# Kernel tuning notes

Hardware: AMD Instinct MI355X
Metric: run time of the kernel (lower is better)

The kernel has to match this reference:

```python
import jax, jax.numpy as jnp
import numpy as np

SEG = 2048      # segment_length
RATE = 4        # dilated_rate
DIM = 768
LN_EPS = 1e-5


def _sparsify(x):
    # b (l s) d -> b l s d, take every RATE-th within segment, flatten back
    b, L, d = x.shape
    x = x.reshape(b, L // SEG, SEG, d)[:, :, ::RATE]
    return x.reshape(b, -1, d)


def _layernorm(x, gamma, beta):
    mu = jnp.mean(x, axis=-1, keepdims=True)
    var = jnp.mean(jnp.square(x - mu), axis=-1, keepdims=True)
    return (x - mu) / jnp.sqrt(var + LN_EPS) * gamma + beta


def setup_inputs() -> dict:
    key = jax.random.key(0)
    ks = jax.random.split(key, 6)
    B, L, D = 4, 8192, DIM
    return {
        "Q": jax.random.normal(ks[0], (B, L, D), dtype=jnp.float32),
        "K": jax.random.normal(ks[1], (B, L, D), dtype=jnp.float32),
        "V": jax.random.normal(ks[2], (B, L, D), dtype=jnp.float32),
        "Wq": jax.random.normal(ks[3], (D, D), dtype=jnp.float32) * (1.0 / np.sqrt(D)),
        "Wk": jax.random.normal(ks[4], (D, D), dtype=jnp.float32) * (1.0 / np.sqrt(D)),
        "Wv": jax.random.normal(ks[5], (D, D), dtype=jnp.float32) * (1.0 / np.sqrt(D)),
        "ln_gamma": jnp.ones((D,), dtype=jnp.float32),
        "ln_beta": jnp.zeros((D,), dtype=jnp.float32),
    }


def reference(Q, K, V, Wq, Wk, Wv, ln_gamma, ln_beta):
    # strided segment dilation gather
    q = _sparsify(Q)  # [B, Ls, D], Ls = L/SEG * ceil(SEG/RATE)
    k = _sparsify(K)
    v = _sparsify(V)
    # linear projections (torch Linear: y = x @ W.T, no bias)
    q = q @ Wq.T
    k = k @ Wk.T
    v = v @ Wv.T
    # qk LayerNorm (shared norm module)
    q = _layernorm(q, ln_gamma, ln_beta)
    k = _layernorm(k, ln_gamma, ln_beta)
    # scaled dot product attention (non-causal, default scale 1/sqrt(D))
    scale = 1.0 / np.sqrt(q.shape[-1]).astype(np.float32)
    attn = jax.nn.softmax(jnp.einsum('bqd,bkd->bqk', q, k) * scale, axis=-1)
    out = jnp.einsum('bqk,bkd->bqd', attn, v)
    # dropout is identity in eval mode; final softmax over feature dim (as in source)
    return jax.nn.softmax(out, axis=-1)
```

## Files before the change

### kernel.cpp

```cpp
#include <hip/hip_runtime.h>
#include <math.h>

#define SEGLEN 2048
#define SRATE 4
#define DIM 768
#define BATCH 4
#define LFULL 8192
#define LSP 2048
#define NROWS (BATCH * LSP)
#define LN_EPS 1e-5f
#define ATT_SCALE 0.03608439182435161f

typedef __attribute__((ext_vector_type(8))) short s16x8;
typedef __attribute__((ext_vector_type(4))) float f32x4;

__device__ __forceinline__ ushort f2bf(float f) {
    unsigned u = __float_as_uint(f);
    u += 0x7fffu + ((u >> 16) & 1u);
    return (ushort)(u >> 16);
}
__device__ __forceinline__ float bf2f(ushort h) {
    return __uint_as_float(((unsigned)h) << 16);
}

__device__ __forceinline__ void ld_lds16(const ushort* g, ushort* l) {
    __builtin_amdgcn_global_load_lds(
        (const __attribute__((address_space(1))) void*)g,
        (__attribute__((address_space(3))) void*)l, 16, 0, 0);
}

__global__ void pack3(const float* __restrict__ Q, const float* __restrict__ Ks,
                      const float* __restrict__ V, ushort* __restrict__ X) {
    const float* src = blockIdx.z == 0 ? Q : blockIdx.z == 1 ? Ks : V;
    ushort* dst = X + (long)blockIdx.z * (NROWS * DIM);
    int idx = blockIdx.x * 256 + threadIdx.x;
    int r  = idx / (DIM / 4);
    int dg = idx - r * (DIM / 4);
    int bb = r >> 11;
    int s  = r & 2047;
    int seg = s >> 9;
    int j   = s & 511;
    long srow = (long)bb * LFULL + seg * SEGLEN + j * SRATE;
    float4 f = *(const float4*)(src + srow * DIM + dg * 4);
    ushort4 o;
    o.x = f2bf(f.x); o.y = f2bf(f.y); o.z = f2bf(f.z); o.w = f2bf(f.w);
    *(ushort4*)(dst + (long)r * DIM + dg * 4) = o;
}

__global__ void conv3(const float* __restrict__ Wq, const float* __restrict__ Wk,
                      const float* __restrict__ Wv, ushort* __restrict__ W) {
    const float* src = blockIdx.z == 0 ? Wq : blockIdx.z == 1 ? Wk : Wv;
    ushort* dst = W + (long)blockIdx.z * (DIM * DIM);
    int idx = blockIdx.x * 256 + threadIdx.x;
    float4 f = *(const float4*)(src + (long)idx * 4);
    ushort4 o;
    o.x = f2bf(f.x); o.y = f2bf(f.y); o.z = f2bf(f.z); o.w = f2bf(f.w);
    *(ushort4*)(dst + (long)idx * 4) = o;
}

template<int MODE>
__global__ __launch_bounds__(512, 2) void gemm8(
    const ushort* __restrict__ Ag, const ushort* __restrict__ Bg,
    ushort* __restrict__ Cb, ushort* __restrict__ Cb2,
    float* __restrict__ Cf, float* __restrict__ Cf2, float* __restrict__ lsum,
    int M, int N, int K, int lda, int ldb, long sA, long sB, long sC,
    int ldc, float scale)
{
    __shared__ ushort lds[2][2][16384];

    const int z = blockIdx.z;
    const int bz = (MODE == 3) ? (z >> 1) : z;
    const int hz = (MODE == 3) ? (z & 1) : 0;
    const ushort* Aop = Ag + (long)bz * sA + (long)hz * K;
    const ushort* Bop = Bg + (long)bz * sB + (long)hz * K;

    const int tid = threadIdx.x;
    const int w = tid >> 6, lane = tid & 63;
    const int wm = w >> 2, wn = w & 3;
    const int quad = lane >> 4, lr = lane & 15;
    const int rowBase = blockIdx.y * 256;
    const int colBase = blockIdx.x * 256;

    int ib = ((lane & 15) << 6) | ((lane >> 4) << 4);
    ib ^= ((ib >> 9) & 1) << 5;

    long offA[4], offB[4];
#pragma unroll
    for (int i = 0; i < 4; i++) {
        int c = i * 512 + tid;
        int cc = c ^ (((c >> 5) & 1) << 1);
        int s = cc >> 6;
        int row  = ((s >> 1) << 4) + ((cc >> 2) & 15);
        int colE = ((s & 1) << 5) + ((cc & 3) << 3);
        offA[i] = (long)(rowBase + row) * lda + colE;
        offB[i] = (long)(colBase + row) * ldb + colE;
    }

    const int NT = K >> 6;

#define STA(buf, vv, i) ld_lds16(Aop + offA[i] + (long)(vv) * 64, &lds[buf][0][(i) * 4096 + w * 512])
#define STB(buf, vv, i) ld_lds16(Bop + offB[i] + (long)(vv) * 64, &lds[buf][1][(i) * 4096 + w * 512])

#pragma unroll
    for (int i = 0; i < 4; i++) STB(0, 0, i);
#pragma unroll
    for (int i = 0; i < 4; i++) STA(0, 0, i);
#pragma unroll
    for (int i = 0; i < 4; i++) STB(1, 1, i);
#pragma unroll
    for (int i = 0; i < 4; i++) STA(1, 1, i);
    asm volatile("s_waitcnt vmcnt(8)" ::: "memory");
    __builtin_amdgcn_s_barrier();

    f32x4 acc[8][4] = {};
    s16x8 bq[4][2];

    for (int v = 0; v < NT; ++v) {
        const int b = v & 1;
        const char* lA = (const char*)&lds[b][0][0];
        const char* lB = (const char*)&lds[b][1][0];
#pragma unroll
        for (int p = 0; p < 4; ++p) {
            s16x8 aq[2][2];
#pragma unroll
            for (int t = 0; t < 2; ++t)
#pragma unroll
                for (int ks = 0; ks < 2; ++ks)
                    aq[t][ks] = *(const s16x8*)(lA + (((wm * 8 + p * 2 + t) * 2 + ks) << 10) + ib);
            if (p == 0) {
#pragma unroll
                for (int n = 0; n < 4; ++n)
#pragma unroll
                    for (int ks = 0; ks < 2; ++ks)
                        bq[n][ks] = *(const s16x8*)(lB + (((wn * 4 + n) * 2 + ks) << 10) + ib);
            }
            if (p == 0 && v >= 1 && v + 1 < NT) { STA(b ^ 1, v + 1, 0); STA(b ^ 1, v + 1, 1); }
            if (p == 1 && v >= 1 && v + 1 < NT) { STA(b ^ 1, v + 1, 2); STA(b ^ 1, v + 1, 3); }
            if (p == 2 && v + 2 < NT)           { STB(b,     v + 2, 0); STB(b,     v + 2, 1); }
            if (p == 3 && v + 2 < NT)           { STB(b,     v + 2, 2); STB(b,     v + 2, 3); }

            __builtin_amdgcn_s_barrier();
            __builtin_amdgcn_s_setprio(1);
#pragma unroll
            for (int t = 0; t < 2; ++t)
#pragma unroll
                for (int n = 0; n < 4; ++n)
#pragma unroll
                    for (int ks = 0; ks < 2; ++ks)
                        acc[p * 2 + t][n] = __builtin_amdgcn_mfma_f32_16x16x32_bf16(
                            aq[t][ks], bq[n][ks], acc[p * 2 + t][n], 0, 0, 0);
            __builtin_amdgcn_s_setprio(0);
            if (p == 3) {
                if (v + 2 < NT)      asm volatile("s_waitcnt vmcnt(4)" ::: "memory");
                else if (v + 1 < NT) asm volatile("s_waitcnt vmcnt(0)" ::: "memory");
            }
            __builtin_amdgcn_s_barrier();
        }
    }
#undef STA
#undef STB

    if (MODE == 0) {
        if (z < 2) {
            ushort* Cz = Cb + (long)z * sC;
#pragma unroll
            for (int i = 0; i < 8; i++) {
                int r0 = rowBase + wm * 128 + i * 16 + quad * 4;
#pragma unroll
                for (int j = 0; j < 4; j++) {
                    int c = colBase + wn * 64 + j * 16 + lr;
#pragma unroll
                    for (int reg = 0; reg < 4; reg++)
                        Cz[(long)(r0 + reg) * ldc + c] = f2bf(acc[i][j][reg]);
                }
            }
        } else {
#pragma unroll
            for (int i = 0; i < 8; i++) {
                int r0 = rowBase + wm * 128 + i * 16 + quad * 4;
                int bidx = r0 >> 11;
                int jj = r0 & 2047;
                ushort* Cz = Cb2 + (long)bidx * DIM * LSP;
#pragma unroll
                for (int j = 0; j < 4; j++) {
                    int c = colBase + wn * 64 + j * 16 + lr;
                    ushort4 o;
                    o.x = f2bf(acc[i][j][0]); o.y = f2bf(acc[i][j][1]);
                    o.z = f2bf(acc[i][j][2]); o.w = f2bf(acc[i][j][3]);
                    *(ushort4*)(Cz + (long)c * LSP + jj) = o;
                }
            }
        }
    } else if (MODE == 2) {
        ushort* Cz = Cb + (long)z * sC;
        float* lz = lsum + (long)z * M;
#pragma unroll
        for (int i = 0; i < 8; i++) {
            int r0 = rowBase + wm * 128 + i * 16 + quad * 4;
#pragma unroll
            for (int reg = 0; reg < 4; reg++) {
                float s = 0.f;
#pragma unroll
                for (int j = 0; j < 4; j++) {
                    int c = colBase + wn * 64 + j * 16 + lr;
                    float e = __expf(acc[i][j][reg] * scale);
                    s += e;
                    Cz[(long)(r0 + reg) * ldc + c] = f2bf(e);
                }
                for (int m = 1; m < 16; m <<= 1) s += __shfl_xor(s, m, 64);
                if (lr == 0) atomicAdd(&lz[r0 + reg], s);
            }
        }
    } else {
        float* Cz = (hz ? Cf2 : Cf) + (long)bz * sC;
#pragma unroll
        for (int i = 0; i < 8; i++) {
            int r0 = rowBase + wm * 128 + i * 16 + quad * 4;
#pragma unroll
            for (int j = 0; j < 4; j++) {
                int c = colBase + wn * 64 + j * 16 + lr;
#pragma unroll
                for (int reg = 0; reg < 4; reg++)
                    Cz[(long)(r0 + reg) * ldc + c] = acc[i][j][reg];
            }
        }
    }
}

__global__ __launch_bounds__(256) void ln_inplace(
    ushort* __restrict__ X, const float* __restrict__ gamma,
    const float* __restrict__ beta)
{
    int wid = threadIdx.x >> 6, lane = threadIdx.x & 63;
    int row = blockIdx.x * 4 + wid;
    ushort* xp = X + (long)row * DIM;
    float v[12];
    float s = 0.f;
#pragma unroll
    for (int c = 0; c < 12; c++) { v[c] = bf2f(xp[c * 64 + lane]); s += v[c]; }
    for (int m = 1; m < 64; m <<= 1) s += __shfl_xor(s, m, 64);
    float mean = s * (1.0f / 768.0f);
    float q = 0.f;
#pragma unroll
    for (int c = 0; c < 12; c++) { float d = v[c] - mean; q += d * d; }
    for (int m = 1; m < 64; m <<= 1) q += __shfl_xor(q, m, 64);
    float rstd = rsqrtf(q * (1.0f / 768.0f) + LN_EPS);
#pragma unroll
    for (int c = 0; c < 12; c++) {
        int idx = c * 64 + lane;
        float y = (v[c] - mean) * rstd * gamma[idx] + beta[idx];
        xp[idx] = f2bf(y);
    }
}

__global__ __launch_bounds__(256) void final_softmax(
    const float* __restrict__ O0, const float* __restrict__ O1,
    const float* __restrict__ l, float* __restrict__ out)
{
    int wid = threadIdx.x >> 6, lane = threadIdx.x & 63;
    int row = blockIdx.x * 4 + wid;
    long base = (long)row * DIM;
    float inv = 1.0f / l[row];
    float v[12]; float mx = -1e30f;
#pragma unroll
    for (int c = 0; c < 12; c++) {
        v[c] = (O0[base + c * 64 + lane] + O1[base + c * 64 + lane]) * inv;
        mx = fmaxf(mx, v[c]);
    }
    for (int m = 1; m < 64; m <<= 1) mx = fmaxf(mx, __shfl_xor(mx, m, 64));
    float s = 0.f;
#pragma unroll
    for (int c = 0; c < 12; c++) { v[c] = __expf(v[c] - mx); s += v[c]; }
    for (int m = 1; m < 64; m <<= 1) s += __shfl_xor(s, m, 64);
    float invs = 1.0f / s;
#pragma unroll
    for (int c = 0; c < 12; c++) out[base + c * 64 + lane] = v[c] * invs;
}

extern "C" void kernel_launch(void* const* d_in, const int* in_sizes, int n_in,
                              void* d_out, int out_size, void* d_ws, size_t ws_size,
                              hipStream_t stream)
{
    const float* Q  = (const float*)d_in[0];
    const float* K_ = (const float*)d_in[1];
    const float* V  = (const float*)d_in[2];
    const float* Wq = (const float*)d_in[3];
    const float* Wk = (const float*)d_in[4];
    const float* Wv = (const float*)d_in[5];
    const float* g  = (const float*)d_in[6];
    const float* b  = (const float*)d_in[7];
    float* out = (float*)d_out;

    char* ws = (char*)d_ws;
    ushort* Xq  = (ushort*)(ws + 0);
    ushort* Wqb = (ushort*)(ws + 37748736);
    ushort* qb  = (ushort*)(ws + 41287680);
    ushort* kb  = (ushort*)(ws + 53870592);
    ushort* vT  = (ushort*)(ws + 66453504);
    float*  O0  = (float*)(ws + 79036416);
    float*  l   = (float*)(ws + 104202240);
    ushort* P   = (ushort*)(ws + 0);
    float*  O1  = (float*)(ws + 41287680);

    (void)in_sizes; (void)n_in; (void)out_size; (void)ws_size;

    hipMemsetAsync(l, 0, NROWS * sizeof(float), stream);

    pack3<<<dim3(6144, 1, 3), 256, 0, stream>>>(Q, K_, V, Xq);
    conv3<<<dim3(576, 1, 3), 256, 0, stream>>>(Wq, Wk, Wv, Wqb);

    gemm8<0><<<dim3(DIM / 256, NROWS / 256, 3), 512, 0, stream>>>(
        Xq, Wqb, qb, vT, nullptr, nullptr, nullptr,
        NROWS, DIM, DIM, DIM, DIM,
        (long)NROWS * DIM, (long)DIM * DIM, (long)NROWS * DIM, DIM, 0.f);

    ln_inplace<<<4096, 256, 0, stream>>>(qb, g, b);

    gemm8<2><<<dim3(LSP / 256, LSP / 256, BATCH), 512, 0, stream>>>(
        qb, kb, P, nullptr, nullptr, nullptr, l,
        LSP, LSP, DIM, DIM, DIM,
        (long)LSP * DIM, (long)LSP * DIM, (long)LSP * LSP, LSP, ATT_SCALE);

    gemm8<3><<<dim3(DIM / 256, LSP / 256, BATCH * 2), 512, 0, stream>>>(
        P, vT, nullptr, nullptr, O0, O1, nullptr,
        LSP, DIM, LSP / 2, LSP, LSP,
        (long)LSP * LSP, (long)DIM * LSP, (long)LSP * DIM, DIM, 0.f);

    final_softmax<<<2048, 256, 0, stream>>>(O0, O1, l, out);
}
```

Before: 395.8 us.

## Shrink GEMM tiles to 128x128 with simpler double buffering and XCD-aware block remap

Replaces the 256x256, 8-wave GEMM tile with a 128x128, 4-wave tile and a simpler pipeline that prefetches the next K-slice at the start of each iteration and waits once at the end. It also remaps the flattened block index round-robin across eight groups, apparently to spread neighbouring tiles across the MI355X's XCDs for L2 locality. The aim is more workgroups to fill the CUs, since the grids were small, and less scheduling complexity. In exchange, each tile reuses data less and does more global and LDS loading per FLOP, and the interleaved A/B prefetch schedule is lost.

```diff
diff --git a/kernel.cpp b/kernel.cpp
--- a/kernel.cpp
+++ b/kernel.cpp
@@ -59,27 +59,35 @@
 }
 
 template<int MODE>
-__global__ __launch_bounds__(512, 2) void gemm8(
+__global__ __launch_bounds__(256, 2) void gemm_bt(
     const ushort* __restrict__ Ag, const ushort* __restrict__ Bg,
     ushort* __restrict__ Cb, ushort* __restrict__ Cb2,
     float* __restrict__ Cf, float* __restrict__ Cf2, float* __restrict__ lsum,
     int M, int N, int K, int lda, int ldb, long sA, long sB, long sC,
     int ldc, float scale)
 {
-    __shared__ ushort lds[2][2][16384];
-
-    const int z = blockIdx.z;
+    __shared__ ushort lds[2][2][8192];
+
+    const int gx = gridDim.x, gy = gridDim.y;
+    const int G = gx * gy * gridDim.z;
+    const int f = blockIdx.x + gx * (blockIdx.y + gy * blockIdx.z);
+    const int wg = (f & 7) * (G >> 3) + (f >> 3);
+    const int bx = wg % gx;
+    const int rest = wg / gx;
+    const int by = rest % gy;
+    const int z  = rest / gy;
+
     const int bz = (MODE == 3) ? (z >> 1) : z;
     const int hz = (MODE == 3) ? (z & 1) : 0;
     const ushort* Aop = Ag + (long)bz * sA + (long)hz * K;
     const ushort* Bop = Bg + (long)bz * sB + (long)hz * K;
 
     const int tid = threadIdx.x;
-    const int w = tid >> 6, lane = tid & 63;
-    const int wm = w >> 2, wn = w & 3;
+    const int wid = tid >> 6, lane = tid & 63;
+    const int wm = wid >> 1, wn = wid & 1;
     const int quad = lane >> 4, lr = lane & 15;
-    const int rowBase = blockIdx.y * 256;
-    const int colBase = blockIdx.x * 256;
+    const int rowBase = by * 128;
+    const int colBase = bx * 128;
 
     int ib = ((lane & 15) << 6) | ((lane >> 4) << 4);
     ib ^= ((ib >> 9) & 1) << 5;
@@ -87,7 +95,7 @@
     long offA[4], offB[4];
 #pragma unroll
     for (int i = 0; i < 4; i++) {
-        int c = i * 512 + tid;
+        int c = i * 256 + tid;
         int cc = c ^ (((c >> 5) & 1) << 1);
         int s = cc >> 6;
         int row  = ((s >> 1) << 4) + ((cc >> 2) & 15);
@@ -98,64 +106,44 @@
 
     const int NT = K >> 6;
 
-#define STA(buf, vv, i) ld_lds16(Aop + offA[i] + (long)(vv) * 64, &lds[buf][0][(i) * 4096 + w * 512])
-#define STB(buf, vv, i) ld_lds16(Bop + offB[i] + (long)(vv) * 64, &lds[buf][1][(i) * 4096 + w * 512])
-
-#pragma unroll
-    for (int i = 0; i < 4; i++) STB(0, 0, i);
-#pragma unroll
-    for (int i = 0; i < 4; i++) STA(0, 0, i);
-#pragma unroll
-    for (int i = 0; i < 4; i++) STB(1, 1, i);
-#pragma unroll
-    for (int i = 0; i < 4; i++) STA(1, 1, i);
-    asm volatile("s_waitcnt vmcnt(8)" ::: "memory");
+#define STA(buf, vv, i) ld_lds16(Aop + offA[i] + (long)(vv) * 64, &lds[buf][0][(i) * 2048 + wid * 512])
+#define STB(buf, vv, i) ld_lds16(Bop + offB[i] + (long)(vv) * 64, &lds[buf][1][(i) * 2048 + wid * 512])
+
+#pragma unroll
+    for (int i = 0; i < 4; i++) { STA(0, 0, i); STB(0, 0, i); }
+    asm volatile("s_waitcnt vmcnt(0)" ::: "memory");
     __builtin_amdgcn_s_barrier();
 
-    f32x4 acc[8][4] = {};
-    s16x8 bq[4][2];
+    f32x4 acc[4][4] = {};
 
     for (int v = 0; v < NT; ++v) {
         const int b = v & 1;
+        if (v + 1 < NT) {
+#pragma unroll
+            for (int i = 0; i < 4; i++) { STA(b ^ 1, v + 1, i); STB(b ^ 1, v + 1, i); }
+        }
         const char* lA = (const char*)&lds[b][0][0];
         const char* lB = (const char*)&lds[b][1][0];
 #pragma unroll
-        for (int p = 0; p < 4; ++p) {
-            s16x8 aq[2][2];
-#pragma unroll
-            for (int t = 0; t < 2; ++t)
-#pragma unroll
-                for (int ks = 0; ks < 2; ++ks)
-                    aq[t][ks] = *(const s16x8*)(lA + (((wm * 8 + p * 2 + t) * 2 + ks) << 10) + ib);
-            if (p == 0) {
-#pragma unroll
-                for (int n = 0; n < 4; ++n)
-#pragma unroll
-                    for (int ks = 0; ks < 2; ++ks)
-                        bq[n][ks] = *(const s16x8*)(lB + (((wn * 4 + n) * 2 + ks) << 10) + ib);
-            }
-            if (p == 0 && v >= 1 && v + 1 < NT) { STA(b ^ 1, v + 1, 0); STA(b ^ 1, v + 1, 1); }
-            if (p == 1 && v >= 1 && v + 1 < NT) { STA(b ^ 1, v + 1, 2); STA(b ^ 1, v + 1, 3); }
-            if (p == 2 && v + 2 < NT)           { STB(b,     v + 2, 0); STB(b,     v + 2, 1); }
-            if (p == 3 && v + 2 < NT)           { STB(b,     v + 2, 2); STB(b,     v + 2, 3); }
-
-            __builtin_amdgcn_s_barrier();
+        for (int ks = 0; ks < 2; ++ks) {
+            s16x8 af[4], bfm[4];
+#pragma unroll
+            for (int t = 0; t < 4; ++t)
+                af[t] = *(const s16x8*)(lA + (((wm * 4 + t) * 2 + ks) << 10) + ib);
+#pragma unroll
+            for (int t = 0; t < 4; ++t)
+                bfm[t] = *(const s16x8*)(lB + (((wn * 4 + t) * 2 + ks) << 10) + ib);
             __builtin_amdgcn_s_setprio(1);
 #pragma unroll
-            for (int t = 0; t < 2; ++t)
-#pragma unroll
-                for (int n = 0; n < 4; ++n)
-#pragma unroll
-                    for (int ks = 0; ks < 2; ++ks)
-                        acc[p * 2 + t][n] = __builtin_amdgcn_mfma_f32_16x16x32_bf16(
-                            aq[t][ks], bq[n][ks], acc[p * 2 + t][n], 0, 0, 0);
+            for (int i = 0; i < 4; i++)
+#pragma unroll
+                for (int j = 0; j < 4; j++)
+                    acc[i][j] = __builtin_amdgcn_mfma_f32_16x16x32_bf16(
+                        af[i], bfm[j], acc[i][j], 0, 0, 0);
             __builtin_amdgcn_s_setprio(0);
-            if (p == 3) {
-                if (v + 2 < NT)      asm volatile("s_waitcnt vmcnt(4)" ::: "memory");
-                else if (v + 1 < NT) asm volatile("s_waitcnt vmcnt(0)" ::: "memory");
-            }
-            __builtin_amdgcn_s_barrier();
-        }
+        }
+        if (v + 1 < NT) asm volatile("s_waitcnt vmcnt(0)" ::: "memory");
+        __builtin_amdgcn_s_barrier();
     }
 #undef STA
 #undef STB
@@ -164,8 +152,8 @@
         if (z < 2) {
             ushort* Cz = Cb + (long)z * sC;
 #pragma unroll
-            for (int i = 0; i < 8; i++) {
-                int r0 = rowBase + wm * 128 + i * 16 + quad * 4;
+            for (int i = 0; i < 4; i++) {
+                int r0 = rowBase + wm * 64 + i * 16 + quad * 4;
 #pragma unroll
                 for (int j = 0; j < 4; j++) {
                     int c = colBase + wn * 64 + j * 16 + lr;
@@ -176,8 +164,8 @@
             }
         } else {
 #pragma unroll
-            for (int i = 0; i < 8; i++) {
-                int r0 = rowBase + wm * 128 + i * 16 + quad * 4;
+            for (int i = 0; i < 4; i++) {
+                int r0 = rowBase + wm * 64 + i * 16 + quad * 4;
                 int bidx = r0 >> 11;
                 int jj = r0 & 2047;
                 ushort* Cz = Cb2 + (long)bidx * DIM * LSP;
@@ -195,8 +183,8 @@
         ushort* Cz = Cb + (long)z * sC;
         float* lz = lsum + (long)z * M;
 #pragma unroll
-        for (int i = 0; i < 8; i++) {
-            int r0 = rowBase + wm * 128 + i * 16 + quad * 4;
+        for (int i = 0; i < 4; i++) {
+            int r0 = rowBase + wm * 64 + i * 16 + quad * 4;
 #pragma unroll
             for (int reg = 0; reg < 4; reg++) {
                 float s = 0.f;
@@ -214,8 +202,8 @@
     } else {
         float* Cz = (hz ? Cf2 : Cf) + (long)bz * sC;
 #pragma unroll
-        for (int i = 0; i < 8; i++) {
-            int r0 = rowBase + wm * 128 + i * 16 + quad * 4;
+        for (int i = 0; i < 4; i++) {
+            int r0 = rowBase + wm * 64 + i * 16 + quad * 4;
 #pragma unroll
             for (int j = 0; j < 4; j++) {
                 int c = colBase + wn * 64 + j * 16 + lr;
@@ -309,19 +297,19 @@
     pack3<<<dim3(6144, 1, 3), 256, 0, stream>>>(Q, K_, V, Xq);
     conv3<<<dim3(576, 1, 3), 256, 0, stream>>>(Wq, Wk, Wv, Wqb);
 
-    gemm8<0><<<dim3(DIM / 256, NROWS / 256, 3), 512, 0, stream>>>(
+    gemm_bt<0><<<dim3(DIM / 128, NROWS / 128, 3), 256, 0, stream>>>(
         Xq, Wqb, qb, vT, nullptr, nullptr, nullptr,
         NROWS, DIM, DIM, DIM, DIM,
         (long)NROWS * DIM, (long)DIM * DIM, (long)NROWS * DIM, DIM, 0.f);
 
     ln_inplace<<<4096, 256, 0, stream>>>(qb, g, b);
 
-    gemm8<2><<<dim3(LSP / 256, LSP / 256, BATCH), 512, 0, stream>>>(
+    gemm_bt<2><<<dim3(LSP / 128, LSP / 128, BATCH), 256, 0, stream>>>(
         qb, kb, P, nullptr, nullptr, nullptr, l,
         LSP, LSP, DIM, DIM, DIM,
         (long)LSP * DIM, (long)LSP * DIM, (long)LSP * LSP, LSP, ATT_SCALE);
 
-    gemm8<3><<<dim3(DIM / 256, LSP / 256, BATCH * 2), 512, 0, stream>>>(
+    gemm_bt<3><<<dim3(DIM / 128, LSP / 128, BATCH * 2), 256, 0, stream>>>(
         P, vT, nullptr, nullptr, O0, O1, nullptr,
         LSP, DIM, LSP / 2, LSP, LSP,
         (long)LSP * LSP, (long)DIM * LSP, (long)LSP * DIM, DIM, 0.f);
```

New measurement: 377.9 us. 1.05x faster.
